# Optimization experiments

Hardware: AMD Instinct MI355X
Metric: run time of the kernel (lower is better)

## Reference

```python
import jax, jax.numpy as jnp
import numpy as np

N, D, P = 8000, 256, 128


def setup_inputs() -> dict:
    key = jax.random.key(0)
    k_adj, k_emb, k_att, k_w, k_f, k_idx = jax.random.split(key, 6)
    # symmetric binary adjacency, avg degree ~ 32, self-loops guarantee deg > 0
    a = (jax.random.uniform(k_adj, (N, N)) < 0.004).astype(jnp.float32)
    adj = jnp.maximum(a, a.T)
    adj = jnp.maximum(adj, jnp.eye(N, dtype=jnp.float32))
    embeddings = jax.random.normal(k_emb, (N, D), dtype=jnp.float32)
    w_att = jax.random.normal(k_att, (D, D), dtype=jnp.float32) / np.sqrt(D)
    b_att = jnp.zeros((D,), dtype=jnp.float32)
    w_weight = jax.random.normal(k_w, (1, 2 * D), dtype=jnp.float32) / np.sqrt(2 * D)
    w_final = jax.random.normal(k_f, (1, 1), dtype=jnp.float32)
    pos_idx = jnp.sort(jax.random.randint(k_idx, (P,), 0, N))  # sorted like torch.nonzero
    return {"adj": adj, "embeddings": embeddings, "w_att": w_att, "b_att": b_att,
            "w_weight": w_weight, "w_final": w_final, "pos_idx": pos_idx}


def reference(adj, embeddings, w_att, b_att, w_weight, w_final, pos_idx):
    n = adj.shape[0]
    # normalized adjacencies (buffers in the torch module)
    dinv = jnp.power(jnp.sum(adj, axis=1), -0.5)          # deg^{-1/2}, [N]
    adj_rcnorm = dinv[None, :] * adj * dinv[:, None]      # d_i^-.5 A_ij d_j^-.5
    adj_rnorm = dinv[None, :] * adj                       # A_ij d_j^-.5
    # one-hot indicator vector (torch forward receives this as `inputs`)
    inputs = jnp.zeros((n,), dtype=adj.dtype).at[pos_idx].set(1.0)
    # gather positive embeddings and adjacency rows (torch.nonzero gather)
    pos_emb = embeddings[pos_idx]                         # [P, D]
    pos_adj = adj[pos_idx]                                # [P, N]
    proj = pos_emb @ w_att.T + b_att                      # [P, D]
    att_scores = pos_adj * (proj @ embeddings.T)          # [P, N], masked scores
    att_probs = jax.nn.softmax(att_scores, axis=0)        # softmax over positives
    context = att_probs.T @ pos_emb                       # [N, D]
    cat = jnp.concatenate([embeddings, context], axis=1)  # [N, 2D]
    mutual_w = jax.nn.sigmoid(cat @ w_weight.T)[:, 0]     # [N]
    # two-hop sparse propagation (expressed as dense matvecs, same math)
    out = adj_rcnorm.T @ inputs                           # [N]
    out = out * mutual_w                                  # elementwise reweight
    out = adj_rnorm.T @ out                               # [N]
    out = out * w_final[0, 0]                             # final Linear(1,1,no bias)
    return out[None, :]                                   # [1, N]
```

## Files before the change

kernel.cpp:

```cpp
#include <hip/hip_runtime.h>
#include <math.h>

#define N 8000
#define D 256
#define P 128
#define NW 250

__global__ __launch_bounds__(256) void deg_kernel(const float* __restrict__ adj,
                                                  float* __restrict__ dinv,
                                                  unsigned int* __restrict__ msk) {
    int row = blockIdx.x;
    int tid = threadIdx.x;
    const float4* r = (const float4*)(adj + (size_t)row * N);
    float s = 0.f;
    if (tid < NW) {
        unsigned int m = 0;
        #pragma unroll
        for (int j = 0; j < 8; j++) {
            float4 a = r[tid * 8 + j];
            s += a.x + a.y + a.z + a.w;
            m |= (a.x != 0.f ? 1u : 0u) << (4 * j + 0);
            m |= (a.y != 0.f ? 1u : 0u) << (4 * j + 1);
            m |= (a.z != 0.f ? 1u : 0u) << (4 * j + 2);
            m |= (a.w != 0.f ? 1u : 0u) << (4 * j + 3);
        }
        msk[(size_t)row * NW + tid] = m;
    }
    for (int off = 32; off > 0; off >>= 1) s += __shfl_down(s, off, 64);
    __shared__ float red[4];
    int lane = tid & 63, wave = tid >> 6;
    if (lane == 0) red[wave] = s;
    __syncthreads();
    if (tid == 0) dinv[row] = rsqrtf(red[0] + red[1] + red[2] + red[3]);
}

__global__ __launch_bounds__(256) void proj_kernel(const float* __restrict__ emb,
                                                   const float* __restrict__ w_att,
                                                   const float* __restrict__ b_att,
                                                   const float* __restrict__ w_weight,
                                                   const int* __restrict__ pos_idx,
                                                   float* __restrict__ projT,
                                                   float* __restrict__ pe2) {
    int p = blockIdx.x;
    int row = pos_idx[p];
    __shared__ float e[D];
    __shared__ float red[D];
    int tid = threadIdx.x;
    e[tid] = emb[(size_t)row * D + tid];
    __syncthreads();
    float acc = b_att[tid];
    const float* wrow = w_att + (size_t)tid * D;
    #pragma unroll 4
    for (int k = 0; k < D; k++) acc += e[k] * wrow[k];
    projT[(size_t)tid * P + p] = acc;
    red[tid] = e[tid] * w_weight[D + tid];
    __syncthreads();
    for (int s = 128; s > 0; s >>= 1) {
        if (tid < s) red[tid] += red[tid + s];
        __syncthreads();
    }
    if (tid == 0) pe2[p] = red[0];
}

__global__ __launch_bounds__(256) void attn_kernel(const float* __restrict__ emb,
                                                   const float* __restrict__ projT,
                                                   const unsigned int* __restrict__ msk,
                                                   const int* __restrict__ pos_idx,
                                                   const float* __restrict__ pe2,
                                                   const float* __restrict__ w_weight,
                                                   const float* __restrict__ dinv,
                                                   float* __restrict__ v) {
    __shared__ float At[32][68];
    __shared__ float B[32][128];
    __shared__ float S[64][129];
    __shared__ float R[16][68];
    __shared__ int   posrow[P];
    __shared__ float pe2s[P];
    __shared__ float fac[P];
    __shared__ float w1[D];

    int tid = threadIdx.x;
    int tx = tid & 15;
    int ty = tid >> 4;
    int n0 = blockIdx.x * 64;

    if (tid < P) {
        int r0 = pos_idx[tid];
        posrow[tid] = r0;
        pe2s[tid] = pe2[tid];
        float f = dinv[r0];
        if (tid > 0 && pos_idx[tid - 1] == r0) f = 0.f;
        fac[tid] = f;
    }
    w1[tid] = w_weight[tid];

    float acc[4][8];
    #pragma unroll
    for (int i = 0; i < 4; i++)
        #pragma unroll
        for (int j = 0; j < 8; j++) acc[i][j] = 0.f;
    float e1 = 0.f;

    for (int d0 = 0; d0 < D; d0 += 32) {
        __syncthreads();
        {
            int nn = tid >> 2;
            int dk0 = (tid & 3) * 8;
            const float* src = emb + (size_t)(n0 + nn) * D + d0 + dk0;
            float4 v0 = *(const float4*)(src);
            float4 v1 = *(const float4*)(src + 4);
            At[dk0 + 0][nn] = v0.x; At[dk0 + 1][nn] = v0.y;
            At[dk0 + 2][nn] = v0.z; At[dk0 + 3][nn] = v0.w;
            At[dk0 + 4][nn] = v1.x; At[dk0 + 5][nn] = v1.y;
            At[dk0 + 6][nn] = v1.z; At[dk0 + 7][nn] = v1.w;
        }
        #pragma unroll
        for (int r = 0; r < 4; r++) {
            int f = (r * 256 + tid) * 4;
            int dk = f >> 7, pp = f & 127;
            *(float4*)&B[dk][pp] = *(const float4*)(projT + (size_t)(d0 + dk) * P + pp);
        }
        __syncthreads();
        #pragma unroll
        for (int dk = 0; dk < 32; dk++) {
            float4 a4 = *(const float4*)&At[dk][tx * 4];
            float b[8];
            *(float4*)&b[0] = *(const float4*)&B[dk][ty * 8];
            *(float4*)&b[4] = *(const float4*)&B[dk][ty * 8 + 4];
            #pragma unroll
            for (int j = 0; j < 8; j++) {
                acc[0][j] += a4.x * b[j];
                acc[1][j] += a4.y * b[j];
                acc[2][j] += a4.z * b[j];
                acc[3][j] += a4.w * b[j];
            }
        }
        if (tid < 64) {
            float t = 0.f;
            #pragma unroll
            for (int dk = 0; dk < 32; dk++) t += At[dk][tid] * w1[d0 + dk];
            e1 += t;
        }
    }

    float vp[4] = {0.f, 0.f, 0.f, 0.f};
    int wbase = (n0 + tx * 4) >> 5;
    int bsh = (tx & 7) * 4;
    #pragma unroll
    for (int j = 0; j < 8; j++) {
        int p = ty * 8 + j;
        unsigned int w = msk[(size_t)posrow[p] * NW + wbase];
        float fp = fac[p];
        float m0 = (w >> (bsh + 0)) & 1u ? 1.f : 0.f;
        float m1 = (w >> (bsh + 1)) & 1u ? 1.f : 0.f;
        float m2 = (w >> (bsh + 2)) & 1u ? 1.f : 0.f;
        float m3 = (w >> (bsh + 3)) & 1u ? 1.f : 0.f;
        S[tx * 4 + 0][p] = acc[0][j] * m0;
        S[tx * 4 + 1][p] = acc[1][j] * m1;
        S[tx * 4 + 2][p] = acc[2][j] * m2;
        S[tx * 4 + 3][p] = acc[3][j] * m3;
        vp[0] += m0 * fp; vp[1] += m1 * fp;
        vp[2] += m2 * fp; vp[3] += m3 * fp;
    }
    #pragma unroll
    for (int i = 0; i < 4; i++) R[ty][tx * 4 + i] = vp[i];
    __syncthreads();

    if (tid < 64) {
        int n = n0 + tid;
        float mm = -1e30f;
        for (int p = 0; p < P; p++) mm = fmaxf(mm, S[tid][p]);
        float Z = 0.f, ape = 0.f;
        for (int p = 0; p < P; p++) {
            float ex = __expf(S[tid][p] - mm);
            Z += ex;
            ape += ex * pe2s[p];
        }
        float vs = 0.f;
        #pragma unroll
        for (int t = 0; t < 16; t++) vs += R[t][tid];
        float logit = e1 + ape / Z;
        float mw = 1.f / (1.f + __expf(-logit));
        v[n] = vs * dinv[n] * mw;
    }
}

__global__ __launch_bounds__(256) void final_kernel(const unsigned int* __restrict__ msk,
                                                    const float* __restrict__ vvec,
                                                    const float* __restrict__ dinv,
                                                    const float* __restrict__ w_final,
                                                    float* __restrict__ out) {
    int wave = threadIdx.x >> 6, lane = threadIdx.x & 63;
    int row = blockIdx.x * 4 + wave;
    const unsigned int* mrow = msk + (size_t)row * NW;
    float s = 0.f;
    for (int wi = lane; wi < NW; wi += 64) {
        unsigned int m = mrow[wi];
        int base = wi * 32;
        while (m) {
            int k = __ffs(m) - 1;
            s += vvec[base + k];
            m &= m - 1;
        }
    }
    for (int off = 32; off > 0; off >>= 1) s += __shfl_down(s, off, 64);
    if (lane == 0) out[row] = s * dinv[row] * w_final[0];
}

extern "C" void kernel_launch(void* const* d_in, const int* in_sizes, int n_in,
                              void* d_out, int out_size, void* d_ws, size_t ws_size,
                              hipStream_t stream) {
    const float* adj    = (const float*)d_in[0];
    const float* emb    = (const float*)d_in[1];
    const float* w_att  = (const float*)d_in[2];
    const float* b_att  = (const float*)d_in[3];
    const float* w_w    = (const float*)d_in[4];
    const float* w_f    = (const float*)d_in[5];
    const int*   pos    = (const int*)d_in[6];
    float* out = (float*)d_out;

    float* ws     = (float*)d_ws;
    float* dinv   = ws;
    float* projT  = dinv + N;
    float* pe2    = projT + (size_t)D * P;
    float* v      = pe2 + P;
    unsigned int* msk = (unsigned int*)(v + N);

    deg_kernel  <<<N,      256, 0, stream>>>(adj, dinv, msk);
    proj_kernel <<<P,      256, 0, stream>>>(emb, w_att, b_att, w_w, pos, projT, pe2);
    attn_kernel <<<N / 64, 256, 0, stream>>>(emb, projT, msk, pos, pe2, w_w, dinv, v);
    final_kernel<<<N / 4,  256, 0, stream>>>(msk, v, dinv, w_f, out);
}
```

Baseline: 407.2 us.

## Merge degree and projection kernels; shrink attention tiles to 32 nodes per block

Combines the degree/mask pass and the positive-embedding projection into one launch, assigning extra blocks to the projection so the two run concurrently and one launch disappears. The attention kernel now handles 32 nodes per block instead of 64, giving 250 blocks rather than 125 so more CUs on the GPU get work. It also loads each positive's mask word once into shared memory and folds the degree-weighted sum into the softmax loop. The cost is a smaller per-thread register tile (4x4), lower arithmetic reuse, and B tiles reloaded by twice as many blocks.

```diff
diff --git a/kernel.cpp b/kernel.cpp
--- a/kernel.cpp
+++ b/kernel.cpp
@@ -6,60 +6,60 @@
 #define P 128
 #define NW 250
 
-__global__ __launch_bounds__(256) void deg_kernel(const float* __restrict__ adj,
-                                                  float* __restrict__ dinv,
-                                                  unsigned int* __restrict__ msk) {
-    int row = blockIdx.x;
-    int tid = threadIdx.x;
-    const float4* r = (const float4*)(adj + (size_t)row * N);
-    float s = 0.f;
-    if (tid < NW) {
-        unsigned int m = 0;
-        #pragma unroll
-        for (int j = 0; j < 8; j++) {
-            float4 a = r[tid * 8 + j];
-            s += a.x + a.y + a.z + a.w;
-            m |= (a.x != 0.f ? 1u : 0u) << (4 * j + 0);
-            m |= (a.y != 0.f ? 1u : 0u) << (4 * j + 1);
-            m |= (a.z != 0.f ? 1u : 0u) << (4 * j + 2);
-            m |= (a.w != 0.f ? 1u : 0u) << (4 * j + 3);
-        }
-        msk[(size_t)row * NW + tid] = m;
-    }
-    for (int off = 32; off > 0; off >>= 1) s += __shfl_down(s, off, 64);
-    __shared__ float red[4];
-    int lane = tid & 63, wave = tid >> 6;
-    if (lane == 0) red[wave] = s;
-    __syncthreads();
-    if (tid == 0) dinv[row] = rsqrtf(red[0] + red[1] + red[2] + red[3]);
-}
-
-__global__ __launch_bounds__(256) void proj_kernel(const float* __restrict__ emb,
+__global__ __launch_bounds__(256) void prep_kernel(const float* __restrict__ adj,
+                                                   const float* __restrict__ emb,
                                                    const float* __restrict__ w_att,
                                                    const float* __restrict__ b_att,
                                                    const float* __restrict__ w_weight,
                                                    const int* __restrict__ pos_idx,
+                                                   float* __restrict__ dinv,
+                                                   unsigned int* __restrict__ msk,
                                                    float* __restrict__ projT,
                                                    float* __restrict__ pe2) {
-    int p = blockIdx.x;
-    int row = pos_idx[p];
-    __shared__ float e[D];
-    __shared__ float red[D];
     int tid = threadIdx.x;
-    e[tid] = emb[(size_t)row * D + tid];
-    __syncthreads();
-    float acc = b_att[tid];
-    const float* wrow = w_att + (size_t)tid * D;
-    #pragma unroll 4
-    for (int k = 0; k < D; k++) acc += e[k] * wrow[k];
-    projT[(size_t)tid * P + p] = acc;
-    red[tid] = e[tid] * w_weight[D + tid];
-    __syncthreads();
-    for (int s = 128; s > 0; s >>= 1) {
-        if (tid < s) red[tid] += red[tid + s];
-        __syncthreads();
-    }
-    if (tid == 0) pe2[p] = red[0];
+    if (blockIdx.x < N) {
+        int row = blockIdx.x;
+        const float4* r = (const float4*)(adj + (size_t)row * N);
+        float s = 0.f;
+        if (tid < NW) {
+            unsigned int m = 0;
+            #pragma unroll
+            for (int j = 0; j < 8; j++) {
+                float4 a = r[tid * 8 + j];
+                s += a.x + a.y + a.z + a.w;
+                m |= (a.x != 0.f ? 1u : 0u) << (4 * j + 0);
+                m |= (a.y != 0.f ? 1u : 0u) << (4 * j + 1);
+                m |= (a.z != 0.f ? 1u : 0u) << (4 * j + 2);
+                m |= (a.w != 0.f ? 1u : 0u) << (4 * j + 3);
+            }
+            msk[(size_t)row * NW + tid] = m;
+        }
+        for (int off = 32; off > 0; off >>= 1) s += __shfl_down(s, off, 64);
+        __shared__ float red4[4];
+        int lane = tid & 63, wave = tid >> 6;
+        if (lane == 0) red4[wave] = s;
+        __syncthreads();
+        if (tid == 0) dinv[row] = rsqrtf(red4[0] + red4[1] + red4[2] + red4[3]);
+    } else {
+        int p = blockIdx.x - N;
+        int row = pos_idx[p];
+        __shared__ float e[D];
+        __shared__ float red[D];
+        e[tid] = emb[(size_t)row * D + tid];
+        __syncthreads();
+        float acc = b_att[tid];
+        const float* wrow = w_att + (size_t)tid * D;
+        #pragma unroll 4
+        for (int k = 0; k < D; k++) acc += e[k] * wrow[k];
+        projT[(size_t)tid * P + p] = acc;
+        red[tid] = e[tid] * w_weight[D + tid];
+        __syncthreads();
+        for (int s = 128; s > 0; s >>= 1) {
+            if (tid < s) red[tid] += red[tid + s];
+            __syncthreads();
+        }
+        if (tid == 0) pe2[p] = red[0];
+    }
 }
 
 __global__ __launch_bounds__(256) void attn_kernel(const float* __restrict__ emb,
@@ -70,19 +70,20 @@
                                                    const float* __restrict__ w_weight,
                                                    const float* __restrict__ dinv,
                                                    float* __restrict__ v) {
-    __shared__ float At[32][68];
+    __shared__ float At[32][36];
     __shared__ float B[32][128];
-    __shared__ float S[64][129];
-    __shared__ float R[16][68];
+    __shared__ float S[32][129];
+    __shared__ unsigned int mword[P];
     __shared__ int   posrow[P];
     __shared__ float pe2s[P];
     __shared__ float fac[P];
     __shared__ float w1[D];
 
     int tid = threadIdx.x;
-    int tx = tid & 15;
-    int ty = tid >> 4;
-    int n0 = blockIdx.x * 64;
+    int tx = tid & 7;
+    int ty = tid >> 3;
+    int n0 = blockIdx.x * 32;
+    int wb = n0 >> 5;
 
     if (tid < P) {
         int r0 = pos_idx[tid];
@@ -94,25 +95,21 @@
     }
     w1[tid] = w_weight[tid];
 
-    float acc[4][8];
+    float acc[4][4];
     #pragma unroll
     for (int i = 0; i < 4; i++)
         #pragma unroll
-        for (int j = 0; j < 8; j++) acc[i][j] = 0.f;
+        for (int j = 0; j < 4; j++) acc[i][j] = 0.f;
     float e1 = 0.f;
 
     for (int d0 = 0; d0 < D; d0 += 32) {
         __syncthreads();
         {
-            int nn = tid >> 2;
-            int dk0 = (tid & 3) * 8;
-            const float* src = emb + (size_t)(n0 + nn) * D + d0 + dk0;
-            float4 v0 = *(const float4*)(src);
-            float4 v1 = *(const float4*)(src + 4);
+            int nn = tid >> 3;
+            int dk0 = (tid & 7) * 4;
+            float4 v0 = *(const float4*)(emb + (size_t)(n0 + nn) * D + d0 + dk0);
             At[dk0 + 0][nn] = v0.x; At[dk0 + 1][nn] = v0.y;
             At[dk0 + 2][nn] = v0.z; At[dk0 + 3][nn] = v0.w;
-            At[dk0 + 4][nn] = v1.x; At[dk0 + 5][nn] = v1.y;
-            At[dk0 + 6][nn] = v1.z; At[dk0 + 7][nn] = v1.w;
         }
         #pragma unroll
         for (int r = 0; r < 4; r++) {
@@ -124,18 +121,17 @@
         #pragma unroll
         for (int dk = 0; dk < 32; dk++) {
             float4 a4 = *(const float4*)&At[dk][tx * 4];
-            float b[8];
-            *(float4*)&b[0] = *(const float4*)&B[dk][ty * 8];
-            *(float4*)&b[4] = *(const float4*)&B[dk][ty * 8 + 4];
-            #pragma unroll
-            for (int j = 0; j < 8; j++) {
-                acc[0][j] += a4.x * b[j];
-                acc[1][j] += a4.y * b[j];
-                acc[2][j] += a4.z * b[j];
-                acc[3][j] += a4.w * b[j];
-            }
-        }
-        if (tid < 64) {
+            float4 b4 = *(const float4*)&B[dk][ty * 4];
+            acc[0][0] += a4.x * b4.x; acc[0][1] += a4.x * b4.y;
+            acc[0][2] += a4.x * b4.z; acc[0][3] += a4.x * b4.w;
+            acc[1][0] += a4.y * b4.x; acc[1][1] += a4.y * b4.y;
+            acc[1][2] += a4.y * b4.z; acc[1][3] += a4.y * b4.w;
+            acc[2][0] += a4.z * b4.x; acc[2][1] += a4.z * b4.y;
+            acc[2][2] += a4.z * b4.z; acc[2][3] += a4.z * b4.w;
+            acc[3][0] += a4.w * b4.x; acc[3][1] += a4.w * b4.y;
+            acc[3][2] += a4.w * b4.z; acc[3][3] += a4.w * b4.w;
+        }
+        if (tid < 32) {
             float t = 0.f;
             #pragma unroll
             for (int dk = 0; dk < 32; dk++) t += At[dk][tid] * w1[d0 + dk];
@@ -143,42 +139,32 @@
         }
     }
 
-    float vp[4] = {0.f, 0.f, 0.f, 0.f};
-    int wbase = (n0 + tx * 4) >> 5;
-    int bsh = (tx & 7) * 4;
+    if (tid < P) mword[tid] = msk[(size_t)posrow[tid] * NW + wb];
+    __syncthreads();
+
     #pragma unroll
-    for (int j = 0; j < 8; j++) {
-        int p = ty * 8 + j;
-        unsigned int w = msk[(size_t)posrow[p] * NW + wbase];
-        float fp = fac[p];
-        float m0 = (w >> (bsh + 0)) & 1u ? 1.f : 0.f;
-        float m1 = (w >> (bsh + 1)) & 1u ? 1.f : 0.f;
-        float m2 = (w >> (bsh + 2)) & 1u ? 1.f : 0.f;
-        float m3 = (w >> (bsh + 3)) & 1u ? 1.f : 0.f;
-        S[tx * 4 + 0][p] = acc[0][j] * m0;
-        S[tx * 4 + 1][p] = acc[1][j] * m1;
-        S[tx * 4 + 2][p] = acc[2][j] * m2;
-        S[tx * 4 + 3][p] = acc[3][j] * m3;
-        vp[0] += m0 * fp; vp[1] += m1 * fp;
-        vp[2] += m2 * fp; vp[3] += m3 * fp;
-    }
-    #pragma unroll
-    for (int i = 0; i < 4; i++) R[ty][tx * 4 + i] = vp[i];
+    for (int j = 0; j < 4; j++) {
+        int p = ty * 4 + j;
+        unsigned int w = mword[p];
+        #pragma unroll
+        for (int i = 0; i < 4; i++) {
+            int nn = tx * 4 + i;
+            S[nn][p] = ((w >> nn) & 1u) ? acc[i][j] : 0.f;
+        }
+    }
     __syncthreads();
 
-    if (tid < 64) {
+    if (tid < 32) {
         int n = n0 + tid;
         float mm = -1e30f;
         for (int p = 0; p < P; p++) mm = fmaxf(mm, S[tid][p]);
-        float Z = 0.f, ape = 0.f;
+        float Z = 0.f, ape = 0.f, vs = 0.f;
         for (int p = 0; p < P; p++) {
             float ex = __expf(S[tid][p] - mm);
             Z += ex;
             ape += ex * pe2s[p];
-        }
-        float vs = 0.f;
-        #pragma unroll
-        for (int t = 0; t < 16; t++) vs += R[t][tid];
+            if ((mword[p] >> tid) & 1u) vs += fac[p];
+        }
         float logit = e1 + ape / Z;
         float mw = 1.f / (1.f + __expf(-logit));
         v[n] = vs * dinv[n] * mw;
@@ -226,8 +212,8 @@
     float* v      = pe2 + P;
     unsigned int* msk = (unsigned int*)(v + N);
 
-    deg_kernel  <<<N,      256, 0, stream>>>(adj, dinv, msk);
-    proj_kernel <<<P,      256, 0, stream>>>(emb, w_att, b_att, w_w, pos, projT, pe2);
-    attn_kernel <<<N / 64, 256, 0, stream>>>(emb, projT, msk, pos, pe2, w_w, dinv, v);
+    prep_kernel <<<N + P,  256, 0, stream>>>(adj, emb, w_att, b_att, w_w, pos,
+                                             dinv, msk, projT, pe2);
+    attn_kernel <<<N / 32, 256, 0, stream>>>(emb, projT, msk, pos, pe2, w_w, dinv, v);
     final_kernel<<<N / 4,  256, 0, stream>>>(msk, v, dinv, w_f, out);
 }
```

Measured after the change: 402.4 us. No clear change (-1.2%).
